# Kernel optimization log

Hardware: AMD Instinct MI355X
Metric: run time of the kernel (lower is better)

The kernel has to match this reference:

```python
import jax, jax.numpy as jnp
import numpy as np

B, S, H = 4, 2048, 1024   # batch, seq_len, hidden_dim
E, D = 8, 1024            # num_experts, expert_dim (== hidden per module structure)
TOP_K = 2


def setup_inputs() -> dict:
    key = jax.random.key(0)
    ks = jax.random.split(key, 8)
    scale_h = 1.0 / np.sqrt(H)
    scale_d = 1.0 / np.sqrt(D)
    return {
        "x": jax.random.normal(ks[0], (B, S, H), dtype=jnp.float32),
        # router linear: hidden -> num_experts
        "w_router": jax.random.normal(ks[1], (H, E), dtype=jnp.float32) * scale_h,
        "b_router": jnp.zeros((E,), dtype=jnp.float32),
        # per-expert linear: hidden -> expert_dim
        "w_experts": jax.random.normal(ks[2], (E, H, D), dtype=jnp.float32) * scale_h,
        "b_experts": jnp.zeros((E, D), dtype=jnp.float32),
        # output linear: expert_dim -> expert_dim
        "w_out": jax.random.normal(ks[3], (D, D), dtype=jnp.float32) * scale_d,
        "b_out": jnp.zeros((D,), dtype=jnp.float32),
    }


def reference(x, w_router, b_router, w_experts, b_experts, w_out, b_out):
    # --- MoERouter: softmax over expert logits, top-2, renormalize ---
    logits = jnp.einsum("bsh,he->bse", x, w_router) + b_router          # [B,S,E]
    probs = jax.nn.softmax(logits, axis=-1)
    top_p, top_i = jax.lax.top_k(probs, TOP_K)                           # [B,S,2]
    top_p = top_p / jnp.sum(top_p, axis=-1, keepdims=True)
    # --- Dense expert compute over all tokens (module computes every expert) ---
    expert_out = jnp.einsum("bsh,ehd->bsed", x, w_experts) + b_experts   # [B,S,E,D]
    expert_out = jax.nn.gelu(expert_out)
    # --- Gather top-2 expert outputs and combine with routing weights ---
    sel = jnp.take_along_axis(expert_out, top_i[..., None], axis=2)      # [B,S,2,D]
    combined = jnp.sum(sel * top_p[..., None], axis=2)                   # [B,S,D]
    # --- Output projection ---
    return jnp.einsum("bsd,de->bse", combined, w_out) + b_out
```

## Files before the change

kernel.cpp:

```cpp
#include <hip/hip_runtime.h>


#define TOKENS 8192
#define HDIM   1024
#define DDIM   1024
#define NEXP   8

typedef __bf16 bf16x8 __attribute__((ext_vector_type(8)));
typedef float  f32x4  __attribute__((ext_vector_type(4)));

__device__ __forceinline__ unsigned short f2b(float f) {
  unsigned int u = __builtin_bit_cast(unsigned int, f);
  u = u + 0x7fffu + ((u >> 16) & 1u);
  return (unsigned short)(u >> 16);
}
__device__ __forceinline__ float b2f(unsigned short b) {
  unsigned int u = ((unsigned int)b) << 16;
  return __builtin_bit_cast(float, u);
}

__device__ __forceinline__ void gld_lds16(const void* g, void* l) {
  __builtin_amdgcn_global_load_lds(
      (__attribute__((address_space(1))) void*)(g),
      (__attribute__((address_space(3))) void*)(l),
      16, 0, 0);
}


__global__ void transpose_cvt_kernel(const float* __restrict__ we, const float* __restrict__ wo,
                                     unsigned short* __restrict__ weT, unsigned short* __restrict__ woT) {
  __shared__ unsigned short tile[32][33];
  int z = blockIdx.z;
  const float* s;
  unsigned short* d;
  if (z < 8) { s = we + (size_t)z * HDIM * DDIM; d = weT + (size_t)z * HDIM * DDIM; }
  else       { s = wo;                            d = woT; }
  int bx = blockIdx.x * 32;
  int by = blockIdx.y * 32;
  for (int i = threadIdx.y; i < 32; i += 8)
    tile[i][threadIdx.x] = f2b(s[(size_t)(by + i) * 1024 + bx + threadIdx.x]);
  __syncthreads();
  for (int i = threadIdx.y; i < 32; i += 8)
    d[(size_t)(bx + i) * 1024 + by + threadIdx.x] = tile[threadIdx.x][i];
}


__global__ void router_compute_kernel(const float* __restrict__ x, const float* __restrict__ wr,
                                      const float* __restrict__ br,
                                      int* __restrict__ eidx, float* __restrict__ ew,
                                      unsigned short* __restrict__ xb) {
  int wave = threadIdx.x >> 6, lane = threadIdx.x & 63;
  int t = blockIdx.x * 4 + wave;
  const float* xp = x + (size_t)t * HDIM;
  unsigned short* xbp = xb + (size_t)t * HDIM;
  float acc[8];
#pragma unroll
  for (int e = 0; e < 8; ++e) acc[e] = 0.f;
#pragma unroll
  for (int h0 = 0; h0 < HDIM; h0 += 256) {
    int h = h0 + lane * 4;
    float4 xv = *(const float4*)&xp[h];
    ushort4 o;
    o.x = f2b(xv.x); o.y = f2b(xv.y); o.z = f2b(xv.z); o.w = f2b(xv.w);
    *(ushort4*)&xbp[h] = o;
    float xq[4] = {xv.x, xv.y, xv.z, xv.w};
#pragma unroll
    for (int q = 0; q < 4; ++q) {
      const float4* wp = (const float4*)&wr[(h + q) * 8];
      float4 w0 = wp[0], w1 = wp[1];
      acc[0] += xq[q] * w0.x; acc[1] += xq[q] * w0.y; acc[2] += xq[q] * w0.z; acc[3] += xq[q] * w0.w;
      acc[4] += xq[q] * w1.x; acc[5] += xq[q] * w1.y; acc[6] += xq[q] * w1.z; acc[7] += xq[q] * w1.w;
    }
  }
#pragma unroll
  for (int off = 32; off; off >>= 1)
#pragma unroll
    for (int e = 0; e < 8; ++e) acc[e] += __shfl_xor(acc[e], off, 64);
  if (lane == 0) {
    float l[8], p[8];
    float m = -1e30f;
#pragma unroll
    for (int e = 0; e < 8; ++e) { l[e] = acc[e] + br[e]; m = fmaxf(m, l[e]); }
    float s = 0.f;
#pragma unroll
    for (int e = 0; e < 8; ++e) { p[e] = __expf(l[e] - m); s += p[e]; }
    int i1 = 0;
#pragma unroll
    for (int e = 1; e < 8; ++e) if (p[e] > p[i1]) i1 = e;
    int i2 = (i1 == 0) ? 1 : 0;
#pragma unroll
    for (int e = 0; e < 8; ++e) if (e != i1 && p[e] > p[i2]) i2 = e;
    float ps = p[i1] + p[i2];
    eidx[t * 2]     = i1;  ew[t * 2]     = p[i1] / ps;
    eidx[t * 2 + 1] = i2;  ew[t * 2 + 1] = p[i2] / ps;
  }
}


__global__ __launch_bounds__(1024) void build_lists_kernel(
    const int* __restrict__ eidx, const float* __restrict__ ew,
    int* __restrict__ counts, int* __restrict__ tok2, float* __restrict__ wl) {
  int e = blockIdx.x;
  int tid = threadIdx.x;
  int lane = tid & 63, wv = tid >> 6;
  __shared__ int wsum[16];
  __shared__ int base;
  if (tid == 0) base = 0;
  __syncthreads();
  for (int c = 0; c < 2 * TOKENS; c += 1024) {
    int i = c + tid;
    bool m = (eidx[i] == e);
    unsigned long long bal = __ballot(m);
    if (lane == 0) wsum[wv] = __popcll(bal);
    __syncthreads();
    int wbase = base;
    for (int w = 0; w < wv; ++w) wbase += wsum[w];
    if (m) {
      int pos = wbase + __popcll(bal & ((1ull << lane) - 1ull));
      tok2[e * TOKENS + pos] = i;
      wl[e * TOKENS + pos] = ew[i];
    }
    int total = 0;
#pragma unroll
    for (int w = 0; w < 16; ++w) total += wsum[w];
    __syncthreads();
    if (tid == 0) base += total;
    __syncthreads();
  }
  if (tid == 0) counts[e] = base;
}


__global__ __launch_bounds__(256, 3) void expert_gemm_kernel(
    const unsigned short* __restrict__ xb, const unsigned short* __restrict__ weT,
    const float* __restrict__ b_experts, const int* __restrict__ counts,
    const int* __restrict__ tok2, const float* __restrict__ wlist,
    unsigned short* __restrict__ outslot) {
  int b = blockIdx.x;
  int id = (b >> 3) + (b & 7) * 512;
  int e = id >> 9;
  int rem = id & 511;
  int m0 = (rem >> 3) << 7;
  int n0 = (rem & 7) << 7;
  int cnt = counts[e];
  if (m0 >= cnt) return;

  __shared__ unsigned short As[3][128 * 32];
  __shared__ unsigned short Bs[3][128 * 32];
  __shared__ int   tokS[128];
  __shared__ float wS[128];

  int tid = threadIdx.x;
  if (tid < 128) {
    int r = m0 + tid;
    tokS[tid] = (r < cnt) ? tok2[e * TOKENS + r] : 0;
    wS[tid]   = (r < cnt) ? wlist[e * TOKENS + r] : 0.f;
  }
  __syncthreads();

  int wave = tid >> 6, lane = tid & 63;
  int subr = lane >> 2, koff = (lane & 3) * 8;

  const unsigned short* wbase = weT + (size_t)e * (HDIM * DDIM);
  const unsigned short* asrc[2];
  const unsigned short* bsrc[2];
  unsigned short* adst[3][2];
  unsigned short* bdst[3][2];
#pragma unroll
  for (int i = 0; i < 2; ++i) {
    int row = i * 64 + wave * 16 + subr;
    asrc[i] = xb + (size_t)(tokS[row] >> 1) * HDIM + koff;
    bsrc[i] = wbase + (size_t)(n0 + row) * HDIM + koff;
#pragma unroll
    for (int bb = 0; bb < 3; ++bb) {
      adst[bb][i] = &As[bb][i * 2048 + wave * 512];
      bdst[bb][i] = &Bs[bb][i * 2048 + wave * 512];
    }
  }

  int wm = wave & 1, wn = wave >> 1;
  int quad = lane >> 4, lr = lane & 15;

  f32x4 zero = {0.f, 0.f, 0.f, 0.f};
  f32x4 acc[4][4];
#pragma unroll
  for (int i = 0; i < 4; ++i)
#pragma unroll
    for (int j = 0; j < 4; ++j) acc[i][j] = zero;

#pragma unroll
  for (int s = 0; s < 2; ++s)
#pragma unroll
    for (int i = 0; i < 2; ++i) {
      gld_lds16(asrc[i] + s * 32, adst[s][i]);
      gld_lds16(bsrc[i] + s * 32, bdst[s][i]);
    }

#pragma unroll
  for (int kk = 0; kk < 32; ++kk) {
    if (kk < 31) asm volatile("s_waitcnt vmcnt(4)" ::: "memory");
    else         asm volatile("s_waitcnt vmcnt(0)" ::: "memory");
    __builtin_amdgcn_s_barrier();
    if (kk + 2 < 32) {
      int nb = (kk + 2) % 3;
      int off = (kk + 2) * 32;
#pragma unroll
      for (int i = 0; i < 2; ++i) {
        gld_lds16(asrc[i] + off, adst[nb][i]);
        gld_lds16(bsrc[i] + off, bdst[nb][i]);
      }
    }
    int cb = kk % 3;
    bf16x8 af[4], bfr[4];
#pragma unroll
    for (int i = 0; i < 4; ++i)
      af[i] = *(const bf16x8*)&As[cb][(wm * 64 + i * 16 + lr) * 32 + quad * 8];
#pragma unroll
    for (int j = 0; j < 4; ++j)
      bfr[j] = *(const bf16x8*)&Bs[cb][(wn * 64 + j * 16 + lr) * 32 + quad * 8];
#pragma unroll
    for (int i = 0; i < 4; ++i)
#pragma unroll
      for (int j = 0; j < 4; ++j)
        acc[i][j] = __builtin_amdgcn_mfma_f32_16x16x32_bf16(af[i], bfr[j], acc[i][j], 0, 0, 0);
  }

#pragma unroll
  for (int j = 0; j < 4; ++j) {
    int col = n0 + wn * 64 + j * 16 + lr;
    float bias = b_experts[e * DDIM + col];
#pragma unroll
    for (int i = 0; i < 4; ++i) {
      int rbase = wm * 64 + i * 16 + quad * 4;
#pragma unroll
      for (int r = 0; r < 4; ++r) {
        int row = rbase + r;
        if (m0 + row < cnt) {
          float h = acc[i][j][r] + bias;
          float z = 0.7978845608f * (h + 0.044715f * h * h * h);
          float t = 1.f - 2.f / (__expf(2.f * z) + 1.f);
          float g = 0.5f * h * (1.f + t);
          outslot[(size_t)tokS[row] * DDIM + col] = f2b(g * wS[row]);
        }
      }
    }
  }
}


__global__ void combine_kernel(const ushort4* __restrict__ outslot, ushort4* __restrict__ comb) {
  int i = blockIdx.x * 256 + threadIdx.x;
  int t = i >> 8, d4 = i & 255;
  ushort4 a = outslot[t * 512 + d4];
  ushort4 b = outslot[t * 512 + 256 + d4];
  ushort4 o;
  o.x = f2b(b2f(a.x) + b2f(b.x));
  o.y = f2b(b2f(a.y) + b2f(b.y));
  o.z = f2b(b2f(a.z) + b2f(b.z));
  o.w = f2b(b2f(a.w) + b2f(b.w));
  comb[i] = o;
}


__global__ __launch_bounds__(256, 3) void out_gemm_kernel(
    const unsigned short* __restrict__ Abf, const unsigned short* __restrict__ BT,
    const float* __restrict__ bias, float* __restrict__ out) {
  int b = blockIdx.x;
  int id = (b >> 3) + (b & 7) * 64;
  int n0 = (id >> 6) << 7;
  int m0 = (id & 63) << 7;

  __shared__ unsigned short As[3][128 * 32];
  __shared__ unsigned short Bs[3][128 * 32];
  int tid = threadIdx.x, wave = tid >> 6, lane = tid & 63;
  int subr = lane >> 2, koff = (lane & 3) * 8;

  const unsigned short* asrc[2];
  const unsigned short* bsrc[2];
  unsigned short* adst[3][2];
  unsigned short* bdst[3][2];
#pragma unroll
  for (int i = 0; i < 2; ++i) {
    int row = i * 64 + wave * 16 + subr;
    asrc[i] = Abf + (size_t)(m0 + row) * DDIM + koff;
    bsrc[i] = BT + (size_t)(n0 + row) * DDIM + koff;
#pragma unroll
    for (int bb = 0; bb < 3; ++bb) {
      adst[bb][i] = &As[bb][i * 2048 + wave * 512];
      bdst[bb][i] = &Bs[bb][i * 2048 + wave * 512];
    }
  }

  int wm = wave & 1, wn = wave >> 1;
  int quad = lane >> 4, lr = lane & 15;

  f32x4 zero = {0.f, 0.f, 0.f, 0.f};
  f32x4 acc[4][4];
#pragma unroll
  for (int i = 0; i < 4; ++i)
#pragma unroll
    for (int j = 0; j < 4; ++j) acc[i][j] = zero;

#pragma unroll
  for (int s = 0; s < 2; ++s)
#pragma unroll
    for (int i = 0; i < 2; ++i) {
      gld_lds16(asrc[i] + s * 32, adst[s][i]);
      gld_lds16(bsrc[i] + s * 32, bdst[s][i]);
    }

#pragma unroll
  for (int kk = 0; kk < 32; ++kk) {
    if (kk < 31) asm volatile("s_waitcnt vmcnt(4)" ::: "memory");
    else         asm volatile("s_waitcnt vmcnt(0)" ::: "memory");
    __builtin_amdgcn_s_barrier();
    if (kk + 2 < 32) {
      int nb = (kk + 2) % 3;
      int off = (kk + 2) * 32;
#pragma unroll
      for (int i = 0; i < 2; ++i) {
        gld_lds16(asrc[i] + off, adst[nb][i]);
        gld_lds16(bsrc[i] + off, bdst[nb][i]);
      }
    }
    int cb = kk % 3;
    bf16x8 af[4], bfr[4];
#pragma unroll
    for (int i = 0; i < 4; ++i)
      af[i] = *(const bf16x8*)&As[cb][(wm * 64 + i * 16 + lr) * 32 + quad * 8];
#pragma unroll
    for (int j = 0; j < 4; ++j)
      bfr[j] = *(const bf16x8*)&Bs[cb][(wn * 64 + j * 16 + lr) * 32 + quad * 8];
#pragma unroll
    for (int i = 0; i < 4; ++i)
#pragma unroll
      for (int j = 0; j < 4; ++j)
        acc[i][j] = __builtin_amdgcn_mfma_f32_16x16x32_bf16(af[i], bfr[j], acc[i][j], 0, 0, 0);
  }

#pragma unroll
  for (int j = 0; j < 4; ++j) {
    int col = n0 + wn * 64 + j * 16 + lr;
    float bs = bias[col];
#pragma unroll
    for (int i = 0; i < 4; ++i) {
      int rbase = wm * 64 + i * 16 + quad * 4;
#pragma unroll
      for (int r = 0; r < 4; ++r)
        out[(size_t)(m0 + rbase + r) * DDIM + col] = acc[i][j][r] + bs;
    }
  }
}


extern "C" void kernel_launch(void* const* d_in, const int* in_sizes, int n_in,
                              void* d_out, int out_size, void* d_ws, size_t ws_size,
                              hipStream_t stream) {
  const float* x  = (const float*)d_in[0];
  const float* wr = (const float*)d_in[1];
  const float* br = (const float*)d_in[2];
  const float* we = (const float*)d_in[3];
  const float* be = (const float*)d_in[4];
  const float* wo = (const float*)d_in[5];
  const float* bo = (const float*)d_in[6];
  float* out = (float*)d_out;

  char* ws = (char*)d_ws;
  unsigned short* xb      = (unsigned short*)(ws);
  unsigned short* weT     = (unsigned short*)(ws + 16777216);
  unsigned short* woT     = (unsigned short*)(ws + 33554432);
  unsigned short* outslot = (unsigned short*)(ws + 35651584);
  int*            counts  = (int*)           (ws + 69206016);
  int*            tok2    = (int*)           (ws + 69206272);
  float*          wlist   = (float*)         (ws + 69468416);
  int*            eidx    = (int*)           (ws + 69730560);
  float*          ew      = (float*)         (ws + 69796096);
  unsigned short* comb    = xb;

  router_compute_kernel<<<2048, 256, 0, stream>>>(x, wr, br, eidx, ew, xb);
  transpose_cvt_kernel<<<dim3(32, 32, 9), dim3(32, 8), 0, stream>>>(we, wo, weT, woT);
  build_lists_kernel<<<8, 1024, 0, stream>>>(eidx, ew, counts, tok2, wlist);
  expert_gemm_kernel<<<4096, 256, 0, stream>>>(xb, weT, be, counts, tok2, wlist, outslot);
  combine_kernel<<<8192, 256, 0, stream>>>((const ushort4*)outslot, (ushort4*)comb);
  out_gemm_kernel<<<512, 256, 0, stream>>>(comb, woT, bo, out);
}
```

Before: 280.0 us.

## Widen expert GEMM tile to 128x256 with 512-thread blocks

Doubles the N-dimension of each expert GEMM block tile from 128 to 256 and uses 8 waves per block instead of 4. Each gathered activation tile is now reused across twice as many output columns, which halves the number of times A rows are fetched. The change adds LDS per block, alters the wait-count pipeline depth, and halves the grid size. That could reduce occupancy and weaken load balance across CUs.

```diff
diff --git a/kernel.cpp b/kernel.cpp
--- a/kernel.cpp
+++ b/kernel.cpp
@@ -131,22 +131,22 @@
 }
 
 
-__global__ __launch_bounds__(256, 3) void expert_gemm_kernel(
+__global__ __launch_bounds__(512, 4) void expert_gemm_kernel(
     const unsigned short* __restrict__ xb, const unsigned short* __restrict__ weT,
     const float* __restrict__ b_experts, const int* __restrict__ counts,
     const int* __restrict__ tok2, const float* __restrict__ wlist,
     unsigned short* __restrict__ outslot) {
   int b = blockIdx.x;
-  int id = (b >> 3) + (b & 7) * 512;
-  int e = id >> 9;
-  int rem = id & 511;
-  int m0 = (rem >> 3) << 7;
-  int n0 = (rem & 7) << 7;
+  int id = (b >> 3) + (b & 7) * 256;
+  int e = id >> 8;
+  int rem = id & 255;
+  int m0 = (rem >> 2) << 7;
+  int n0 = (rem & 3) << 8;
   int cnt = counts[e];
   if (m0 >= cnt) return;
 
   __shared__ unsigned short As[3][128 * 32];
-  __shared__ unsigned short Bs[3][128 * 32];
+  __shared__ unsigned short Bs[3][256 * 32];
   __shared__ int   tokS[128];
   __shared__ float wS[128];
 
@@ -159,26 +159,25 @@
   __syncthreads();
 
   int wave = tid >> 6, lane = tid & 63;
-  int subr = lane >> 2, koff = (lane & 3) * 8;
+  int srow = tid >> 2, koff = (tid & 3) * 8;
 
   const unsigned short* wbase = weT + (size_t)e * (HDIM * DDIM);
-  const unsigned short* asrc[2];
+  const unsigned short* asrc = xb + (size_t)(tokS[srow] >> 1) * HDIM + koff;
   const unsigned short* bsrc[2];
-  unsigned short* adst[3][2];
+  unsigned short* adst[3];
   unsigned short* bdst[3][2];
 #pragma unroll
-  for (int i = 0; i < 2; ++i) {
-    int row = i * 64 + wave * 16 + subr;
-    asrc[i] = xb + (size_t)(tokS[row] >> 1) * HDIM + koff;
-    bsrc[i] = wbase + (size_t)(n0 + row) * HDIM + koff;
-#pragma unroll
-    for (int bb = 0; bb < 3; ++bb) {
-      adst[bb][i] = &As[bb][i * 2048 + wave * 512];
-      bdst[bb][i] = &Bs[bb][i * 2048 + wave * 512];
-    }
-  }
-
-  int wm = wave & 1, wn = wave >> 1;
+  for (int i = 0; i < 2; ++i)
+    bsrc[i] = wbase + (size_t)(n0 + i * 128 + srow) * HDIM + koff;
+#pragma unroll
+  for (int bb = 0; bb < 3; ++bb) {
+    adst[bb] = &As[bb][wave * 512];
+#pragma unroll
+    for (int i = 0; i < 2; ++i)
+      bdst[bb][i] = &Bs[bb][i * 4096 + wave * 512];
+  }
+
+  int wm = wave >> 2, wn = wave & 3;
   int quad = lane >> 4, lr = lane & 15;
 
   f32x4 zero = {0.f, 0.f, 0.f, 0.f};
@@ -189,26 +188,25 @@
     for (int j = 0; j < 4; ++j) acc[i][j] = zero;
 
 #pragma unroll
-  for (int s = 0; s < 2; ++s)
-#pragma unroll
-    for (int i = 0; i < 2; ++i) {
-      gld_lds16(asrc[i] + s * 32, adst[s][i]);
+  for (int s = 0; s < 2; ++s) {
+    gld_lds16(asrc + s * 32, adst[s]);
+#pragma unroll
+    for (int i = 0; i < 2; ++i)
       gld_lds16(bsrc[i] + s * 32, bdst[s][i]);
-    }
+  }
 
 #pragma unroll
   for (int kk = 0; kk < 32; ++kk) {
-    if (kk < 31) asm volatile("s_waitcnt vmcnt(4)" ::: "memory");
+    if (kk < 31) asm volatile("s_waitcnt vmcnt(3)" ::: "memory");
     else         asm volatile("s_waitcnt vmcnt(0)" ::: "memory");
     __builtin_amdgcn_s_barrier();
     if (kk + 2 < 32) {
       int nb = (kk + 2) % 3;
       int off = (kk + 2) * 32;
-#pragma unroll
-      for (int i = 0; i < 2; ++i) {
-        gld_lds16(asrc[i] + off, adst[nb][i]);
+      gld_lds16(asrc + off, adst[nb]);
+#pragma unroll
+      for (int i = 0; i < 2; ++i)
         gld_lds16(bsrc[i] + off, bdst[nb][i]);
-      }
     }
     int cb = kk % 3;
     bf16x8 af[4], bfr[4];
@@ -380,7 +378,7 @@
   router_compute_kernel<<<2048, 256, 0, stream>>>(x, wr, br, eidx, ew, xb);
   transpose_cvt_kernel<<<dim3(32, 32, 9), dim3(32, 8), 0, stream>>>(we, wo, weT, woT);
   build_lists_kernel<<<8, 1024, 0, stream>>>(eidx, ew, counts, tok2, wlist);
-  expert_gemm_kernel<<<4096, 256, 0, stream>>>(xb, weT, be, counts, tok2, wlist, outslot);
+  expert_gemm_kernel<<<2048, 512, 0, stream>>>(xb, weT, be, counts, tok2, wlist, outslot);
   combine_kernel<<<8192, 256, 0, stream>>>((const ushort4*)outslot, (ushort4*)comb);
   out_gemm_kernel<<<512, 256, 0, stream>>>(comb, woT, bo, out);
 }
```

After: 280.8 us. Within noise of the previous version (+0.3%).

## Write expert GEMM outputs contiguously per expert and gather in combine

Applied to the files above, without the earlier changes.

The expert GEMM epilogue used to scatter each output row to a per-token slot. It now writes rows contiguously in expert-sorted order, using a prefix sum of the expert counts. build_lists records each slot's position (s2p, stored in place over ew), and the combine kernel uses it to gather the two rows per token. This turns scattered stores into coalesced contiguous stores, at the cost of an indirect read in combine and reusing the ew buffer as s2p.

```diff
diff --git a/kernel.cpp b/kernel.cpp
--- a/kernel.cpp
+++ b/kernel.cpp
@@ -98,8 +98,9 @@
 
 
 __global__ __launch_bounds__(1024) void build_lists_kernel(
-    const int* __restrict__ eidx, const float* __restrict__ ew,
-    int* __restrict__ counts, int* __restrict__ tok2, float* __restrict__ wl) {
+    const int* __restrict__ eidx, const float* ew,
+    int* __restrict__ counts, int* __restrict__ tok2, float* __restrict__ wl,
+    int* s2p) {
   int e = blockIdx.x;
   int tid = threadIdx.x;
   int lane = tid & 63, wv = tid >> 6;
@@ -117,8 +118,10 @@
     for (int w = 0; w < wv; ++w) wbase += wsum[w];
     if (m) {
       int pos = wbase + __popcll(bal & ((1ull << lane) - 1ull));
+      float w = ew[i];
       tok2[e * TOKENS + pos] = i;
-      wl[e * TOKENS + pos] = ew[i];
+      wl[e * TOKENS + pos] = w;
+      s2p[i] = pos;
     }
     int total = 0;
 #pragma unroll
@@ -135,7 +138,7 @@
     const unsigned short* __restrict__ xb, const unsigned short* __restrict__ weT,
     const float* __restrict__ b_experts, const int* __restrict__ counts,
     const int* __restrict__ tok2, const float* __restrict__ wlist,
-    unsigned short* __restrict__ outslot) {
+    unsigned short* __restrict__ outE) {
   int b = blockIdx.x;
   int id = (b >> 3) + (b & 7) * 512;
   int e = id >> 9;
@@ -144,6 +147,8 @@
   int n0 = (rem & 7) << 7;
   int cnt = counts[e];
   if (m0 >= cnt) return;
+  int cbase = 0;
+  for (int q = 0; q < e; ++q) cbase += counts[q];
 
   __shared__ unsigned short As[3][128 * 32];
   __shared__ unsigned short Bs[3][128 * 32];
@@ -225,6 +230,7 @@
         acc[i][j] = __builtin_amdgcn_mfma_f32_16x16x32_bf16(af[i], bfr[j], acc[i][j], 0, 0, 0);
   }
 
+  int rowbase = cbase + m0;
 #pragma unroll
   for (int j = 0; j < 4; ++j) {
     int col = n0 + wn * 64 + j * 16 + lr;
@@ -240,7 +246,7 @@
           float z = 0.7978845608f * (h + 0.044715f * h * h * h);
           float t = 1.f - 2.f / (__expf(2.f * z) + 1.f);
           float g = 0.5f * h * (1.f + t);
-          outslot[(size_t)tokS[row] * DDIM + col] = f2b(g * wS[row]);
+          outE[(size_t)(rowbase + row) * DDIM + col] = f2b(g * wS[row]);
         }
       }
     }
@@ -248,17 +254,31 @@
 }
 
 
-__global__ void combine_kernel(const ushort4* __restrict__ outslot, ushort4* __restrict__ comb) {
-  int i = blockIdx.x * 256 + threadIdx.x;
-  int t = i >> 8, d4 = i & 255;
-  ushort4 a = outslot[t * 512 + d4];
-  ushort4 b = outslot[t * 512 + 256 + d4];
+__global__ void combine_kernel(const ushort4* __restrict__ outE,
+                               const int* __restrict__ eidx, const int* __restrict__ s2p,
+                               const int* __restrict__ counts,
+                               ushort4* __restrict__ comb) {
+  __shared__ int cbase[8];
+  int tid = threadIdx.x;
+  if (tid < 8) {
+    int s = 0;
+    for (int q = 0; q < tid; ++q) s += counts[q];
+    cbase[tid] = s;
+  }
+  __syncthreads();
+  int t = blockIdx.x;
+  int d4 = tid;
+  int i0 = t * 2, i1 = i0 + 1;
+  size_t r0 = ((size_t)(cbase[eidx[i0]] + s2p[i0])) * 256 + d4;
+  size_t r1 = ((size_t)(cbase[eidx[i1]] + s2p[i1])) * 256 + d4;
+  ushort4 a = outE[r0];
+  ushort4 b = outE[r1];
   ushort4 o;
   o.x = f2b(b2f(a.x) + b2f(b.x));
   o.y = f2b(b2f(a.y) + b2f(b.y));
   o.z = f2b(b2f(a.z) + b2f(b.z));
   o.w = f2b(b2f(a.w) + b2f(b.w));
-  comb[i] = o;
+  comb[t * 256 + d4] = o;
 }
 
 
@@ -369,18 +389,19 @@
   unsigned short* xb      = (unsigned short*)(ws);
   unsigned short* weT     = (unsigned short*)(ws + 16777216);
   unsigned short* woT     = (unsigned short*)(ws + 33554432);
-  unsigned short* outslot = (unsigned short*)(ws + 35651584);
+  unsigned short* outE    = (unsigned short*)(ws + 35651584);
   int*            counts  = (int*)           (ws + 69206016);
   int*            tok2    = (int*)           (ws + 69206272);
   float*          wlist   = (float*)         (ws + 69468416);
   int*            eidx    = (int*)           (ws + 69730560);
   float*          ew      = (float*)         (ws + 69796096);
+  int*            s2p     = (int*)ew;
   unsigned short* comb    = xb;
 
   router_compute_kernel<<<2048, 256, 0, stream>>>(x, wr, br, eidx, ew, xb);
   transpose_cvt_kernel<<<dim3(32, 32, 9), dim3(32, 8), 0, stream>>>(we, wo, weT, woT);
-  build_lists_kernel<<<8, 1024, 0, stream>>>(eidx, ew, counts, tok2, wlist);
-  expert_gemm_kernel<<<4096, 256, 0, stream>>>(xb, weT, be, counts, tok2, wlist, outslot);
-  combine_kernel<<<8192, 256, 0, stream>>>((const ushort4*)outslot, (ushort4*)comb);
+  build_lists_kernel<<<8, 1024, 0, stream>>>(eidx, ew, counts, tok2, wlist, s2p);
+  expert_gemm_kernel<<<4096, 256, 0, stream>>>(xb, weT, be, counts, tok2, wlist, outE);
+  combine_kernel<<<8192, 256, 0, stream>>>((const ushort4*)outE, eidx, s2p, counts, (ushort4*)comb);
   out_gemm_kernel<<<512, 256, 0, stream>>>(comb, woT, bo, out);
 }
```

Measured after the change: 282.3 us. No clear change (+0.8%).

## Merge router and weight transpose into one launch; vectorize list building

Applied to the files above, without the earlier changes.

Folds the router/bf16 conversion kernel and the weight transpose-convert kernel into a single launch, with block ranges picking the role, so the two independent jobs run concurrently and one launch plus its inter-kernel gap goes away. Rewrites build_lists to load four expert indices and weights per thread with int4/float4 loads, using four ballots per iteration. This cuts its serial loop from 16 iterations to 4, each with three barriers. The order of entries in each expert's list changes but stays deterministic. A dead assignment to the lane mask is left in the code.

```diff
diff --git a/kernel.cpp b/kernel.cpp
--- a/kernel.cpp
+++ b/kernel.cpp
@@ -27,29 +27,34 @@
 }
 
 
-__global__ void transpose_cvt_kernel(const float* __restrict__ we, const float* __restrict__ wo,
-                                     unsigned short* __restrict__ weT, unsigned short* __restrict__ woT) {
+__global__ __launch_bounds__(256) void pre_kernel(
+    const float* __restrict__ x, const float* __restrict__ wr,
+    const float* __restrict__ br,
+    const float* __restrict__ we, const float* __restrict__ wo,
+    unsigned short* __restrict__ weT, unsigned short* __restrict__ woT,
+    unsigned short* __restrict__ xb,
+    int* __restrict__ eidx, float* __restrict__ ew) {
   __shared__ unsigned short tile[32][33];
-  int z = blockIdx.z;
-  const float* s;
-  unsigned short* d;
-  if (z < 8) { s = we + (size_t)z * HDIM * DDIM; d = weT + (size_t)z * HDIM * DDIM; }
-  else       { s = wo;                            d = woT; }
-  int bx = blockIdx.x * 32;
-  int by = blockIdx.y * 32;
-  for (int i = threadIdx.y; i < 32; i += 8)
-    tile[i][threadIdx.x] = f2b(s[(size_t)(by + i) * 1024 + bx + threadIdx.x]);
-  __syncthreads();
-  for (int i = threadIdx.y; i < 32; i += 8)
-    d[(size_t)(bx + i) * 1024 + by + threadIdx.x] = tile[threadIdx.x][i];
-}
-
-
-__global__ void router_compute_kernel(const float* __restrict__ x, const float* __restrict__ wr,
-                                      const float* __restrict__ br,
-                                      int* __restrict__ eidx, float* __restrict__ ew,
-                                      unsigned short* __restrict__ xb) {
-  int wave = threadIdx.x >> 6, lane = threadIdx.x & 63;
+  int tid = threadIdx.x;
+  if (blockIdx.x >= 2048) {
+    int lid = blockIdx.x - 2048;
+    int z = lid >> 10;
+    int rem = lid & 1023;
+    int bx = (rem & 31) * 32;
+    int by = (rem >> 5) * 32;
+    const float* s;
+    unsigned short* d;
+    if (z < 8) { s = we + (size_t)z * HDIM * DDIM; d = weT + (size_t)z * HDIM * DDIM; }
+    else       { s = wo;                            d = woT; }
+    int tx = tid & 31, ty = tid >> 5;
+    for (int i = ty; i < 32; i += 8)
+      tile[i][tx] = f2b(s[(size_t)(by + i) * 1024 + bx + tx]);
+    __syncthreads();
+    for (int i = ty; i < 32; i += 8)
+      d[(size_t)(bx + i) * 1024 + by + tx] = tile[tx][i];
+    return;
+  }
+  int wave = tid >> 6, lane = tid & 63;
   int t = blockIdx.x * 4 + wave;
   const float* xp = x + (size_t)t * HDIM;
   unsigned short* xbp = xb + (size_t)t * HDIM;
@@ -98,7 +103,7 @@
 
 
 __global__ __launch_bounds__(1024) void build_lists_kernel(
-    const int* __restrict__ eidx, const float* __restrict__ ew,
+    const int4* __restrict__ eidx4, const float4* __restrict__ ew4,
     int* __restrict__ counts, int* __restrict__ tok2, float* __restrict__ wl) {
   int e = blockIdx.x;
   int tid = threadIdx.x;
@@ -107,19 +112,32 @@
   __shared__ int base;
   if (tid == 0) base = 0;
   __syncthreads();
-  for (int c = 0; c < 2 * TOKENS; c += 1024) {
-    int i = c + tid;
-    bool m = (eidx[i] == e);
-    unsigned long long bal = __ballot(m);
-    if (lane == 0) wsum[wv] = __popcll(bal);
+#pragma unroll
+  for (int c = 0; c < 4; ++c) {
+    int v4 = c * 1024 + tid;
+    int4   ev = eidx4[v4];
+    float4 fw = ew4[v4];
+    bool m0 = (ev.x == e), m1 = (ev.y == e), m2 = (ev.z == e), m3 = (ev.w == e);
+    unsigned long long b0 = __ballot(m0);
+    unsigned long long b1 = __ballot(m1);
+    unsigned long long b2 = __ballot(m2);
+    unsigned long long b3 = __ballot(m3);
+    int c0 = __popcll(b0), c1 = __popcll(b1), c2 = __popcll(b2), c3 = __popcll(b3);
+    if (lane == 0) wsum[wv] = c0 + c1 + c2 + c3;
     __syncthreads();
     int wbase = base;
     for (int w = 0; w < wv; ++w) wbase += wsum[w];
-    if (m) {
-      int pos = wbase + __popcll(bal & ((1ull << lane) - 1ull));
-      tok2[e * TOKENS + pos] = i;
-      wl[e * TOKENS + pos] = ew[i];
-    }
+    unsigned long long lm = (lane == 63) ? ~0ull >> 1 : (1ull << lane) - 1ull;
+    lm = (1ull << lane) - 1ull;
+    int ibase = c * 4096 + tid * 4;
+    int off0 = wbase;
+    int off1 = off0 + c0;
+    int off2 = off1 + c1;
+    int off3 = off2 + c2;
+    if (m0) { int p = off0 + __popcll(b0 & lm); tok2[e * TOKENS + p] = ibase + 0; wl[e * TOKENS + p] = fw.x; }
+    if (m1) { int p = off1 + __popcll(b1 & lm); tok2[e * TOKENS + p] = ibase + 1; wl[e * TOKENS + p] = fw.y; }
+    if (m2) { int p = off2 + __popcll(b2 & lm); tok2[e * TOKENS + p] = ibase + 2; wl[e * TOKENS + p] = fw.z; }
+    if (m3) { int p = off3 + __popcll(b3 & lm); tok2[e * TOKENS + p] = ibase + 3; wl[e * TOKENS + p] = fw.w; }
     int total = 0;
 #pragma unroll
     for (int w = 0; w < 16; ++w) total += wsum[w];
@@ -377,9 +395,10 @@
   float*          ew      = (float*)         (ws + 69796096);
   unsigned short* comb    = xb;
 
-  router_compute_kernel<<<2048, 256, 0, stream>>>(x, wr, br, eidx, ew, xb);
-  transpose_cvt_kernel<<<dim3(32, 32, 9), dim3(32, 8), 0, stream>>>(we, wo, weT, woT);
-  build_lists_kernel<<<8, 1024, 0, stream>>>(eidx, ew, counts, tok2, wlist);
+  pre_kernel<<<2048 + 9216, 256, 0, stream>>>(x, wr, br, we, wo, weT, woT,
+                                              xb, eidx, ew);
+  build_lists_kernel<<<8, 1024, 0, stream>>>((const int4*)eidx, (const float4*)ew,
+                                             counts, tok2, wlist);
   expert_gemm_kernel<<<4096, 256, 0, stream>>>(xb, weT, be, counts, tok2, wlist, outslot);
   combine_kernel<<<8192, 256, 0, stream>>>((const ushort4*)outslot, (ushort4*)comb);
   out_gemm_kernel<<<512, 256, 0, stream>>>(comb, woT, bo, out);
```

Result: faster. 260.7 us (-6.9%).
